# Kernel optimization log

Measured on AMD Instinct MI355X. Metric: run time of the kernel, lower is better.

Reference implementation:

```python
import jax, jax.numpy as jnp
import numpy as np

N = 100000
NNZ = 3200000
K = 3

def setup_inputs() -> dict:
    key = jax.random.key(0)
    ks = jax.random.split(key, 9)
    return {
        "x": jax.random.normal(ks[0], (N, 128), dtype=jnp.float32),
        "vals": jax.random.uniform(ks[1], (NNZ,), dtype=jnp.float32) * (1.0 / 32.0),
        "W1": jax.random.normal(ks[2], (128 * K, 256), dtype=jnp.float32) * 0.05,
        "b1": jax.random.normal(ks[3], (256,), dtype=jnp.float32) * 0.05,
        "W2": jax.random.normal(ks[4], (256 * K, 64), dtype=jnp.float32) * 0.05,
        "b2": jax.random.normal(ks[5], (64,), dtype=jnp.float32) * 0.05,
        "rows": jax.random.randint(ks[6], (NNZ,), 0, N, dtype=jnp.int32),
        "cols": jax.random.randint(ks[7], (NNZ,), 0, N, dtype=jnp.int32),
        "idx": jax.random.randint(ks[8], (50000,), 0, N, dtype=jnp.int32),
    }

def _spmm(rows, cols, vals, x):
    # sparse [N,N] @ dense [N,F] via gather + segment_sum
    return jax.ops.segment_sum(vals[:, None] * x[cols], rows, num_segments=N)

def _cheb_basis(x, rows, cols, vals, k):
    # Chebyshev recurrence: T0=x, T1=L x, T_m = 2 L T_{m-1} - T_{m-2}
    xs = [x]
    if k > 1:
        x0, x1 = x, _spmm(rows, cols, vals, x)
        xs.append(x1)
        for _ in range(2, k):
            x2 = 2.0 * _spmm(rows, cols, vals, x1) - x0
            xs.append(x2)
            x0, x1 = x1, x2
    # match torch layout: [N, F, K] -> [N, F*K] (per-feature K contiguous)
    return jnp.stack(xs, axis=2).reshape(x.shape[0], -1)

def reference(x, vals, W1, b1, W2, b2, rows, cols, idx):
    h = _cheb_basis(x, rows, cols, vals, K) @ W1 + b1
    h = jax.nn.relu(h)  # dropout omitted (eval mode)
    out = _cheb_basis(h, rows, cols, vals, K) @ W2 + b2
    return out[idx]
```

## Files before the change

kernel.cpp:

```cpp
#include <hip/hip_runtime.h>
#include <hip/hip_bf16.h>

typedef __attribute__((ext_vector_type(8))) __bf16 bf16x8;
typedef __attribute__((ext_vector_type(4))) float floatx4;
typedef unsigned short ushort_t;
typedef unsigned int uint_t;

#define N_NODES 100000
#define NNZ_E   3200000
#define N_IDX   50000
#define NB_BKT  196
#define PTILE   8192
#define PBLOCKS 391

__device__ __forceinline__ float bf2f(uint_t u16) {
  union { float f; uint_t i; } v; v.i = u16 << 16; return v.f;
}
__device__ __forceinline__ unsigned short f2bf(float f) {
  union { float f; uint_t i; } v; v.f = f;
  uint_t x = v.i;
  return (unsigned short)((x + 0x7FFFu + ((x >> 16) & 1u)) >> 16);
}


__global__ __launch_bounds__(256) void k_bhist(const int* __restrict__ rows,
                                               int* __restrict__ bcnt) {
  __shared__ int h[NB_BKT];
  for (int i = threadIdx.x; i < NB_BKT; i += 256) h[i] = 0;
  __syncthreads();
  int base = blockIdx.x * PTILE;
  for (int i = threadIdx.x; i < PTILE; i += 256) {
    int e = base + i;
    if (e < NNZ_E) atomicAdd(&h[rows[e] >> 9], 1);
  }
  __syncthreads();
  for (int i = threadIdx.x; i < NB_BKT; i += 256)
    if (h[i]) atomicAdd(&bcnt[i], h[i]);
}

__global__ void k_bscan(const int* __restrict__ bcnt, int* __restrict__ bbase,
                        int* __restrict__ bcur) {
  __shared__ int ts[256];
  int t = threadIdx.x;
  int v = (t < NB_BKT) ? bcnt[t] : 0;
  ts[t] = v;
  __syncthreads();
  for (int off = 1; off < 256; off <<= 1) {
    int x = ts[t];
    int a = (t >= off) ? ts[t - off] : 0;
    __syncthreads();
    ts[t] = x + a;
    __syncthreads();
  }
  if (t < NB_BKT) {
    int b = (t == 0) ? 0 : ts[t - 1];
    bbase[t] = b;
    bcur[t] = b;
  }
}

__global__ __launch_bounds__(256) void k_part(const int* __restrict__ rows,
                                              const int* __restrict__ cols,
                                              const float* __restrict__ vals,
                                              int* __restrict__ bcur,
                                              int2* __restrict__ tmp) {
  __shared__ int h[NB_BKT];
  for (int i = threadIdx.x; i < NB_BKT; i += 256) h[i] = 0;
  __syncthreads();
  int base = blockIdx.x * PTILE;
  for (int i = threadIdx.x; i < PTILE; i += 256) {
    int e = base + i;
    if (e < NNZ_E) atomicAdd(&h[rows[e] >> 9], 1);
  }
  __syncthreads();
  for (int i = threadIdx.x; i < NB_BKT; i += 256) {
    int c = h[i];
    h[i] = c ? atomicAdd(&bcur[i], c) : 0;
  }
  __syncthreads();
  for (int i = threadIdx.x; i < PTILE; i += 256) {
    int e = base + i;
    if (e < NNZ_E) {
      int rr = rows[e];
      int p = atomicAdd(&h[rr >> 9], 1);
      int2 o;
      o.x = cols[e] | ((rr & 511) << 17);
      o.y = __float_as_int(vals[e]);
      tmp[p] = o;
    }
  }
}

__global__ __launch_bounds__(512) void k_sort(const int* __restrict__ bbase,
                                              const int2* __restrict__ tmp,
                                              int2* __restrict__ edges,
                                              int* __restrict__ rowptr) {
  __shared__ int cnt[512];
  __shared__ int ts[512];
  int b = blockIdx.x, t = threadIdx.x;
  int s = bbase[b];
  int epos = (b == NB_BKT - 1) ? NNZ_E : bbase[b + 1];
  cnt[t] = 0;
  __syncthreads();
  for (int i = s + t; i < epos; i += 512)
    atomicAdd(&cnt[(tmp[i].x >> 17) & 511], 1);
  __syncthreads();
  ts[t] = cnt[t];
  __syncthreads();
  for (int off = 1; off < 512; off <<= 1) {
    int x = ts[t];
    int a = (t >= off) ? ts[t - off] : 0;
    __syncthreads();
    ts[t] = x + a;
    __syncthreads();
  }
  int pre = (t == 0) ? 0 : ts[t - 1];
  int grow = b * 512 + t;
  if (grow < N_NODES) rowptr[grow] = s + pre;
  cnt[t] = s + pre;
  __syncthreads();
  for (int i = s + t; i < epos; i += 512) {
    int2 p = tmp[i];
    int rl = (p.x >> 17) & 511;
    int pos = atomicAdd(&cnt[rl], 1);
    int2 o;
    o.x = p.x & 0x1FFFF;
    o.y = p.y;
    edges[pos] = o;
  }
  if (b == 0 && t == 0) rowptr[N_NODES] = NNZ_E;
}


__global__ void k_cvt(const float4* __restrict__ x, ushort4* __restrict__ xb) {
  int i = blockIdx.x * blockDim.x + threadIdx.x;
  if (i < N_NODES * 128 / 4) {
    float4 v = x[i];
    ushort4 o;
    o.x = f2bf(v.x); o.y = f2bf(v.y); o.z = f2bf(v.z); o.w = f2bf(v.w);
    xb[i] = o;
  }
}


__global__ void k_prepW1(const float* __restrict__ W, ushort_t* __restrict__ Wp) {
  int kp = blockIdx.x;
  int n  = threadIdx.x;
  int ch = kp >> 7;
  int f  = kp & 127;
  float v;
  if (ch == 0)      v = W[(f*3+0)*256+n] - W[(f*3+2)*256+n];
  else if (ch == 1) v = W[(f*3+1)*256+n];
  else              v = 2.0f * W[(f*3+2)*256+n];
  int kb = kp >> 5, kr = kp & 31;
  int lane = ((kr >> 3) << 4) | (n & 15);
  Wp[(((size_t)kb * 16 + (n >> 4)) * 64 + lane) * 8 + (kr & 7)] = f2bf(v);
}

__global__ void k_prepW2(const float* __restrict__ W, ushort_t* __restrict__ Wp) {
  int f = blockIdx.x;
  int c = threadIdx.x;
  int g = c >> 6, n = c & 63;
  float v;
  if (g == 0)      v = W[(f*3+0)*64+n] - W[(f*3+2)*64+n];
  else if (g == 1) v = W[(f*3+1)*64+n];
  else             v = 2.0f * W[(f*3+2)*64+n];
  int kb = f >> 5, kr = f & 31;
  int nb = c >> 4;
  int lane = ((kr >> 3) << 4) | (c & 15);
  Wp[(((size_t)kb * 12 + nb) * 64 + lane) * 8 + (kr & 7)] = f2bf(v);
}


__global__ __launch_bounds__(256) void k_spmm128(
    const int* __restrict__ rowptr, const int2* __restrict__ edges,
    const ushort_t* __restrict__ in, ushort_t* __restrict__ out) {
  int r = __builtin_amdgcn_readfirstlane(blockIdx.x * 4 + (threadIdx.x >> 6));
  int f = threadIdx.x & 63;
  int e0 = rowptr[r], e1 = rowptr[r + 1];
  float a0 = 0.f, a1 = 0.f;
  int e = e0;
  for (; e + 16 <= e1; e += 16) {
    int2 E[16];
#pragma unroll
    for (int j = 0; j < 16; ++j) E[j] = edges[e + j];
    uint_t q[16];
#pragma unroll
    for (int j = 0; j < 16; ++j)
      q[j] = *(const uint_t*)(in + (size_t)E[j].x * 128 + 2 * f);
#pragma unroll
    for (int j = 0; j < 16; ++j) {
      float v = __int_as_float(E[j].y);
      a0 = fmaf(v, bf2f(q[j] & 0xFFFFu), a0);
      a1 = fmaf(v, bf2f(q[j] >> 16), a1);
    }
  }
  for (; e + 4 <= e1; e += 4) {
    int2 E[4];
#pragma unroll
    for (int j = 0; j < 4; ++j) E[j] = edges[e + j];
    uint_t q[4];
#pragma unroll
    for (int j = 0; j < 4; ++j)
      q[j] = *(const uint_t*)(in + (size_t)E[j].x * 128 + 2 * f);
#pragma unroll
    for (int j = 0; j < 4; ++j) {
      float v = __int_as_float(E[j].y);
      a0 = fmaf(v, bf2f(q[j] & 0xFFFFu), a0);
      a1 = fmaf(v, bf2f(q[j] >> 16), a1);
    }
  }
  for (; e < e1; ++e) {
    int2 E = edges[e];
    uint_t q = *(const uint_t*)(in + (size_t)E.x * 128 + 2 * f);
    float v = __int_as_float(E.y);
    a0 = fmaf(v, bf2f(q & 0xFFFFu), a0);
    a1 = fmaf(v, bf2f(q >> 16), a1);
  }
  uint_t o = ((uint_t)f2bf(a1) << 16) | (uint_t)f2bf(a0);
  *(uint_t*)(out + (size_t)r * 128 + 2 * f) = o;
}


__global__ __launch_bounds__(256) void k_spmm64_add(
    const int* __restrict__ rowptr, const int2* __restrict__ edges,
    const ushort_t* __restrict__ p2, const ushort_t* __restrict__ p1,
    ushort_t* __restrict__ u) {
  int r = __builtin_amdgcn_readfirstlane(blockIdx.x * 4 + (threadIdx.x >> 6));
  int f = threadIdx.x & 63;
  int e0 = rowptr[r], e1 = rowptr[r + 1];
  float a = 0.f;
  int e = e0;
  for (; e + 16 <= e1; e += 16) {
    int2 E[16];
#pragma unroll
    for (int j = 0; j < 16; ++j) E[j] = edges[e + j];
    ushort_t q[16];
#pragma unroll
    for (int j = 0; j < 16; ++j) q[j] = p2[(size_t)E[j].x * 64 + f];
#pragma unroll
    for (int j = 0; j < 16; ++j)
      a = fmaf(__int_as_float(E[j].y), bf2f(q[j]), a);
  }
  for (; e + 4 <= e1; e += 4) {
    int2 E[4];
#pragma unroll
    for (int j = 0; j < 4; ++j) E[j] = edges[e + j];
    ushort_t q[4];
#pragma unroll
    for (int j = 0; j < 4; ++j) q[j] = p2[(size_t)E[j].x * 64 + f];
#pragma unroll
    for (int j = 0; j < 4; ++j)
      a = fmaf(__int_as_float(E[j].y), bf2f(q[j]), a);
  }
  for (; e < e1; ++e) {
    int2 E = edges[e];
    a = fmaf(__int_as_float(E.y), bf2f(p2[(size_t)E.x * 64 + f]), a);
  }
  float b = a + bf2f(p1[(size_t)r * 64 + f]);
  u[(size_t)r * 64 + f] = f2bf(b);
}


__global__ __launch_bounds__(256) void k_spmm64_idx(
    const int* __restrict__ rowptr, const int2* __restrict__ edges,
    const ushort_t* __restrict__ u, const float* __restrict__ p0,
    const int* __restrict__ idx, float* __restrict__ out) {
  int o = __builtin_amdgcn_readfirstlane(blockIdx.x * 4 + (threadIdx.x >> 6));
  int f = threadIdx.x & 63;
  int r = __builtin_amdgcn_readfirstlane(idx[o]);
  int e0 = rowptr[r], e1 = rowptr[r + 1];
  float a = 0.f;
  int e = e0;
  for (; e + 16 <= e1; e += 16) {
    int2 E[16];
#pragma unroll
    for (int j = 0; j < 16; ++j) E[j] = edges[e + j];
    ushort_t q[16];
#pragma unroll
    for (int j = 0; j < 16; ++j) q[j] = u[(size_t)E[j].x * 64 + f];
#pragma unroll
    for (int j = 0; j < 16; ++j)
      a = fmaf(__int_as_float(E[j].y), bf2f(q[j]), a);
  }
  for (; e + 4 <= e1; e += 4) {
    int2 E[4];
#pragma unroll
    for (int j = 0; j < 4; ++j) E[j] = edges[e + j];
    ushort_t q[4];
#pragma unroll
    for (int j = 0; j < 4; ++j) q[j] = u[(size_t)E[j].x * 64 + f];
#pragma unroll
    for (int j = 0; j < 4; ++j)
      a = fmaf(__int_as_float(E[j].y), bf2f(q[j]), a);
  }
  for (; e < e1; ++e) {
    int2 E = edges[e];
    a = fmaf(__int_as_float(E.y), bf2f(u[(size_t)E.x * 64 + f]), a);
  }
  float res = p0[(size_t)r * 64 + f] + a;
  out[(size_t)o * 64 + f] = res;
}


__global__ __launch_bounds__(256) void k_gemm1(
    const ushort_t* __restrict__ A0, const ushort_t* __restrict__ A1,
    const ushort_t* __restrict__ A2, const ushort_t* __restrict__ Bp,
    const float* __restrict__ bias, ushort_t* __restrict__ h) {
  int lane = threadIdx.x & 63;
  int ng = threadIdx.x >> 6;
  int r0 = blockIdx.x * 64;
  int mrl = lane & 15;
  int ko = (lane >> 4) << 3;
  floatx4 acc[4][4] = {};
#pragma unroll
  for (int kbg = 0; kbg < 12; ++kbg) {
    int c = kbg >> 2, kb = kbg & 3;
    const ushort_t* Asrc = (c == 0 ? A0 : c == 1 ? A1 : A2);
    bf16x8 a[4];
#pragma unroll
    for (int mi = 0; mi < 4; ++mi) {
      int mr = r0 + mi * 16 + mrl;
      if (mr > N_NODES - 1) mr = N_NODES - 1;
      a[mi] = *(const bf16x8*)(Asrc + (size_t)mr * 128 + kb * 32 + ko);
    }
    const ushort_t* Bb = Bp + (((size_t)(kbg * 16 + ng * 4)) * 64 + lane) * 8;
#pragma unroll
    for (int nt = 0; nt < 4; ++nt) {
      bf16x8 b = *(const bf16x8*)(Bb + (size_t)nt * 64 * 8);
#pragma unroll
      for (int mi = 0; mi < 4; ++mi)
        acc[mi][nt] = __builtin_amdgcn_mfma_f32_16x16x32_bf16(a[mi], b, acc[mi][nt], 0, 0, 0);
    }
  }
  int col0 = ng * 64 + (lane & 15);
  int rr0 = (lane >> 4) << 2;
#pragma unroll
  for (int nt = 0; nt < 4; ++nt) {
    int col = col0 + nt * 16;
    float bv = bias[col];
#pragma unroll
    for (int mi = 0; mi < 4; ++mi) {
      int rb = r0 + mi * 16 + rr0;
#pragma unroll
      for (int rg = 0; rg < 4; ++rg) {
        int row = rb + rg;
        if (row < N_NODES) {
          float v = acc[mi][nt][rg] + bv;
          v = v > 0.f ? v : 0.f;
          h[(size_t)row * 256 + col] = f2bf(v);
        }
      }
    }
  }
}


__global__ __launch_bounds__(256) void k_gemm2(
    const ushort_t* __restrict__ A, const ushort_t* __restrict__ Bp,
    const float* __restrict__ bias, float* __restrict__ p0,
    ushort_t* __restrict__ p1, ushort_t* __restrict__ p2) {
  int wid = (blockIdx.x * 256 + threadIdx.x) >> 6;
  int lane = threadIdx.x & 63;
  int mt4 = wid / 3, ng = wid - mt4 * 3;
  if (mt4 >= 1563) return;
  int r0 = mt4 * 64;
  int mrl = lane & 15;
  int ko = (lane >> 4) << 3;
  floatx4 acc[4][4] = {};
#pragma unroll
  for (int kb = 0; kb < 8; ++kb) {
    bf16x8 a[4];
#pragma unroll
    for (int mi = 0; mi < 4; ++mi) {
      int mr = r0 + mi * 16 + mrl;
      if (mr > N_NODES - 1) mr = N_NODES - 1;
      a[mi] = *(const bf16x8*)(A + (size_t)mr * 256 + kb * 32 + ko);
    }
    const ushort_t* Bb = Bp + (((size_t)(kb * 12 + ng * 4)) * 64 + lane) * 8;
#pragma unroll
    for (int nt = 0; nt < 4; ++nt) {
      bf16x8 b = *(const bf16x8*)(Bb + (size_t)nt * 64 * 8);
#pragma unroll
      for (int mi = 0; mi < 4; ++mi)
        acc[mi][nt] = __builtin_amdgcn_mfma_f32_16x16x32_bf16(a[mi], b, acc[mi][nt], 0, 0, 0);
    }
  }
  int c16 = lane & 15;
  int rr0 = (lane >> 4) << 2;
  if (ng == 0) {
#pragma unroll
    for (int nt = 0; nt < 4; ++nt) {
      float bv = bias[nt * 16 + c16];
#pragma unroll
      for (int mi = 0; mi < 4; ++mi) {
        int rb = r0 + mi * 16 + rr0;
#pragma unroll
        for (int rg = 0; rg < 4; ++rg) {
          int row = rb + rg;
          if (row < N_NODES)
            p0[(size_t)row * 64 + nt * 16 + c16] = acc[mi][nt][rg] + bv;
        }
      }
    }
  } else {
    ushort_t* dst = (ng == 1) ? p1 : p2;
#pragma unroll
    for (int nt = 0; nt < 4; ++nt)
#pragma unroll
      for (int mi = 0; mi < 4; ++mi) {
        int rb = r0 + mi * 16 + rr0;
#pragma unroll
        for (int rg = 0; rg < 4; ++rg) {
          int row = rb + rg;
          if (row < N_NODES)
            dst[(size_t)row * 64 + nt * 16 + c16] = f2bf(acc[mi][nt][rg]);
        }
      }
  }
}


extern "C" void kernel_launch(void* const* d_in, const int* in_sizes, int n_in,
                              void* d_out, int out_size, void* d_ws, size_t ws_size,
                              hipStream_t stream) {
  const float* x    = (const float*)d_in[0];
  const float* vals = (const float*)d_in[1];
  const float* W1   = (const float*)d_in[2];
  const float* b1   = (const float*)d_in[3];
  const float* W2   = (const float*)d_in[4];
  const float* b2   = (const float*)d_in[5];
  const int*   rows = (const int*)d_in[6];
  const int*   cols = (const int*)d_in[7];
  const int*   idx  = (const int*)d_in[8];
  float* out = (float*)d_out;

  char* w = (char*)d_ws;
  size_t off = 0;
  auto take = [&](size_t b) -> char* {
    char* p = w + off;
    off += (b + 255) & ~(size_t)255;
    return p;
  };
  int*      bcnt    = (int*)take((size_t)NB_BKT * 4);
  int*      bbase   = (int*)take((size_t)NB_BKT * 4);
  int*      bcur    = (int*)take((size_t)NB_BKT * 4);
  int*      rowptr  = (int*)take((size_t)(N_NODES + 1) * 4);
  int2*     tmp     = (int2*)take((size_t)NNZ_E * 8);
  int2*     edges   = (int2*)take((size_t)NNZ_E * 8);
  ushort_t* xb      = (ushort_t*)take((size_t)N_NODES * 128 * 2);
  ushort_t* T1a     = (ushort_t*)take((size_t)N_NODES * 128 * 2);
  ushort_t* U1      = (ushort_t*)take((size_t)N_NODES * 128 * 2);
  ushort_t* h       = (ushort_t*)take((size_t)N_NODES * 256 * 2);
  ushort_t* W1p     = (ushort_t*)take((size_t)384 * 256 * 2);
  ushort_t* W2p     = (ushort_t*)take((size_t)256 * 192 * 2);

  float*    p0 = (float*)xb;
  ushort_t* p1 = T1a;
  ushort_t* p2 = T1a + (size_t)N_NODES * 64;
  ushort_t* u  = U1;

  hipMemsetAsync(bcnt, 0, (size_t)NB_BKT * 4, stream);
  k_bhist<<<PBLOCKS, 256, 0, stream>>>(rows, bcnt);
  k_bscan<<<1, 256, 0, stream>>>(bcnt, bbase, bcur);
  k_part<<<PBLOCKS, 256, 0, stream>>>(rows, cols, vals, bcur, tmp);
  k_sort<<<NB_BKT, 512, 0, stream>>>(bbase, tmp, edges, rowptr);

  k_cvt<<<(N_NODES * 128 / 4 + 255) / 256, 256, 0, stream>>>((const float4*)x, (ushort4*)xb);
  k_prepW1<<<384, 256, 0, stream>>>(W1, W1p);
  k_prepW2<<<256, 192, 0, stream>>>(W2, W2p);

  k_spmm128<<<N_NODES / 4, 256, 0, stream>>>(rowptr, edges, xb, T1a);
  k_spmm128<<<N_NODES / 4, 256, 0, stream>>>(rowptr, edges, T1a, U1);
  k_gemm1<<<1563, 256, 0, stream>>>(xb, T1a, U1, W1p, b1, h);

  k_gemm2<<<1173, 256, 0, stream>>>(h, W2p, b2, p0, p1, p2);
  k_spmm64_add<<<N_NODES / 4, 256, 0, stream>>>(rowptr, edges, p2, p1, u);
  k_spmm64_idx<<<N_IDX / 4, 256, 0, stream>>>(rowptr, edges, u, p0, idx, out);
}
```

Measured before the change: 672.1 us.

## Replace two-pass bucket sort with per-row counting sort and fuse prep kernels

Builds the CSR with a per-row histogram using global atomics, a two-level scan, and a direct atomic scatter into the edges array. This removes the temporary buffer and the second local sort pass. The three conversion and weight-prep kernels are merged into one launch to cut launch overhead. The trade-off is heavy global atomic contention on row counters and fully scattered edge writes, with edge order within a row now nondeterministic.

Result: slower. 830.7 us (+23.6%).

```diff
diff --git a/kernel.cpp b/kernel.cpp
--- a/kernel.cpp
+++ b/kernel.cpp
@@ -10,8 +10,7 @@
 #define NNZ_E   3200000
 #define N_IDX   50000
 #define NB_BKT  196
-#define PTILE   8192
-#define PBLOCKS 391
+#define NROW_PAD (NB_BKT * 512)
 
 __device__ __forceinline__ float bf2f(uint_t u16) {
   union { float f; uint_t i; } v; v.i = u16 << 16; return v.f;
@@ -23,19 +22,27 @@
 }
 
 
-__global__ __launch_bounds__(256) void k_bhist(const int* __restrict__ rows,
-                                               int* __restrict__ bcnt) {
-  __shared__ int h[NB_BKT];
-  for (int i = threadIdx.x; i < NB_BKT; i += 256) h[i] = 0;
+__global__ __launch_bounds__(256) void k_rhist(const int4* __restrict__ rows,
+                                               int* __restrict__ rcnt) {
+  int i = blockIdx.x * 256 + threadIdx.x;
+  int4 r = rows[i];
+  atomicAdd(&rcnt[r.x], 1);
+  atomicAdd(&rcnt[r.y], 1);
+  atomicAdd(&rcnt[r.z], 1);
+  atomicAdd(&rcnt[r.w], 1);
+}
+
+__global__ __launch_bounds__(512) void k_rscan1(const int* __restrict__ rcnt,
+                                                int* __restrict__ bsum) {
+  __shared__ int s[512];
+  int t = threadIdx.x;
+  s[t] = rcnt[blockIdx.x * 512 + t];
   __syncthreads();
-  int base = blockIdx.x * PTILE;
-  for (int i = threadIdx.x; i < PTILE; i += 256) {
-    int e = base + i;
-    if (e < NNZ_E) atomicAdd(&h[rows[e] >> 9], 1);
-  }
-  __syncthreads();
-  for (int i = threadIdx.x; i < NB_BKT; i += 256)
-    if (h[i]) atomicAdd(&bcnt[i], h[i]);
+  for (int off = 256; off > 0; off >>= 1) {
+    if (t < off) s[t] += s[t + off];
+    __syncthreads();
+  }
+  if (t == 0) bsum[blockIdx.x] = s[0];
 }
 
 __global__ void k_bscan(const int* __restrict__ bcnt, int* __restrict__ bbase,
@@ -59,53 +66,14 @@
   }
 }
 
-__global__ __launch_bounds__(256) void k_part(const int* __restrict__ rows,
-                                              const int* __restrict__ cols,
-                                              const float* __restrict__ vals,
-                                              int* __restrict__ bcur,
-                                              int2* __restrict__ tmp) {
-  __shared__ int h[NB_BKT];
-  for (int i = threadIdx.x; i < NB_BKT; i += 256) h[i] = 0;
-  __syncthreads();
-  int base = blockIdx.x * PTILE;
-  for (int i = threadIdx.x; i < PTILE; i += 256) {
-    int e = base + i;
-    if (e < NNZ_E) atomicAdd(&h[rows[e] >> 9], 1);
-  }
-  __syncthreads();
-  for (int i = threadIdx.x; i < NB_BKT; i += 256) {
-    int c = h[i];
-    h[i] = c ? atomicAdd(&bcur[i], c) : 0;
-  }
-  __syncthreads();
-  for (int i = threadIdx.x; i < PTILE; i += 256) {
-    int e = base + i;
-    if (e < NNZ_E) {
-      int rr = rows[e];
-      int p = atomicAdd(&h[rr >> 9], 1);
-      int2 o;
-      o.x = cols[e] | ((rr & 511) << 17);
-      o.y = __float_as_int(vals[e]);
-      tmp[p] = o;
-    }
-  }
-}
-
-__global__ __launch_bounds__(512) void k_sort(const int* __restrict__ bbase,
-                                              const int2* __restrict__ tmp,
-                                              int2* __restrict__ edges,
-                                              int* __restrict__ rowptr) {
-  __shared__ int cnt[512];
+__global__ __launch_bounds__(512) void k_rscan2(const int* __restrict__ rcnt,
+                                                const int* __restrict__ bbase,
+                                                int* __restrict__ rowptr,
+                                                int* __restrict__ cur) {
   __shared__ int ts[512];
   int b = blockIdx.x, t = threadIdx.x;
-  int s = bbase[b];
-  int epos = (b == NB_BKT - 1) ? NNZ_E : bbase[b + 1];
-  cnt[t] = 0;
-  __syncthreads();
-  for (int i = s + t; i < epos; i += 512)
-    atomicAdd(&cnt[(tmp[i].x >> 17) & 511], 1);
-  __syncthreads();
-  ts[t] = cnt[t];
+  int g = b * 512 + t;
+  ts[t] = rcnt[g];
   __syncthreads();
   for (int off = 1; off < 512; off <<= 1) {
     int x = ts[t];
@@ -115,60 +83,69 @@
     __syncthreads();
   }
   int pre = (t == 0) ? 0 : ts[t - 1];
-  int grow = b * 512 + t;
-  if (grow < N_NODES) rowptr[grow] = s + pre;
-  cnt[t] = s + pre;
-  __syncthreads();
-  for (int i = s + t; i < epos; i += 512) {
-    int2 p = tmp[i];
-    int rl = (p.x >> 17) & 511;
-    int pos = atomicAdd(&cnt[rl], 1);
-    int2 o;
-    o.x = p.x & 0x1FFFF;
-    o.y = p.y;
-    edges[pos] = o;
-  }
-  if (b == 0 && t == 0) rowptr[N_NODES] = NNZ_E;
-}
-
-
-__global__ void k_cvt(const float4* __restrict__ x, ushort4* __restrict__ xb) {
-  int i = blockIdx.x * blockDim.x + threadIdx.x;
-  if (i < N_NODES * 128 / 4) {
+  int base = bbase[b] + pre;
+  if (g <= N_NODES) rowptr[g] = base;
+  if (g < N_NODES) cur[g] = base;
+}
+
+__global__ __launch_bounds__(256) void k_rscatter(const int4* __restrict__ rows,
+                                                  const int4* __restrict__ cols,
+                                                  const float4* __restrict__ vals,
+                                                  int* __restrict__ cur,
+                                                  int2* __restrict__ edges) {
+  int i = blockIdx.x * 256 + threadIdx.x;
+  int4 r = rows[i];
+  int4 c = cols[i];
+  float4 v = vals[i];
+  int p0 = atomicAdd(&cur[r.x], 1);
+  int p1 = atomicAdd(&cur[r.y], 1);
+  int p2 = atomicAdd(&cur[r.z], 1);
+  int p3 = atomicAdd(&cur[r.w], 1);
+  edges[p0] = make_int2(c.x, __float_as_int(v.x));
+  edges[p1] = make_int2(c.y, __float_as_int(v.y));
+  edges[p2] = make_int2(c.z, __float_as_int(v.z));
+  edges[p3] = make_int2(c.w, __float_as_int(v.w));
+}
+
+
+__global__ __launch_bounds__(256) void k_prep(
+    const float4* __restrict__ x, const float* __restrict__ W1,
+    const float* __restrict__ W2, ushort4* __restrict__ xb,
+    ushort_t* __restrict__ W1p, ushort_t* __restrict__ W2p) {
+  int b = blockIdx.x;
+  if (b < 12500) {
+    int i = b * 256 + threadIdx.x;
     float4 v = x[i];
     ushort4 o;
     o.x = f2bf(v.x); o.y = f2bf(v.y); o.z = f2bf(v.z); o.w = f2bf(v.w);
     xb[i] = o;
-  }
-}
-
-
-__global__ void k_prepW1(const float* __restrict__ W, ushort_t* __restrict__ Wp) {
-  int kp = blockIdx.x;
-  int n  = threadIdx.x;
-  int ch = kp >> 7;
-  int f  = kp & 127;
-  float v;
-  if (ch == 0)      v = W[(f*3+0)*256+n] - W[(f*3+2)*256+n];
-  else if (ch == 1) v = W[(f*3+1)*256+n];
-  else              v = 2.0f * W[(f*3+2)*256+n];
-  int kb = kp >> 5, kr = kp & 31;
-  int lane = ((kr >> 3) << 4) | (n & 15);
-  Wp[(((size_t)kb * 16 + (n >> 4)) * 64 + lane) * 8 + (kr & 7)] = f2bf(v);
-}
-
-__global__ void k_prepW2(const float* __restrict__ W, ushort_t* __restrict__ Wp) {
-  int f = blockIdx.x;
-  int c = threadIdx.x;
-  int g = c >> 6, n = c & 63;
-  float v;
-  if (g == 0)      v = W[(f*3+0)*64+n] - W[(f*3+2)*64+n];
-  else if (g == 1) v = W[(f*3+1)*64+n];
-  else             v = 2.0f * W[(f*3+2)*64+n];
-  int kb = f >> 5, kr = f & 31;
-  int nb = c >> 4;
-  int lane = ((kr >> 3) << 4) | (c & 15);
-  Wp[(((size_t)kb * 12 + nb) * 64 + lane) * 8 + (kr & 7)] = f2bf(v);
+  } else if (b < 12884) {
+    int kp = b - 12500;
+    int n  = threadIdx.x;
+    int ch = kp >> 7;
+    int f  = kp & 127;
+    float v;
+    if (ch == 0)      v = W1[(f*3+0)*256+n] - W1[(f*3+2)*256+n];
+    else if (ch == 1) v = W1[(f*3+1)*256+n];
+    else              v = 2.0f * W1[(f*3+2)*256+n];
+    int kb = kp >> 5, kr = kp & 31;
+    int lane = ((kr >> 3) << 4) | (n & 15);
+    W1p[(((size_t)kb * 16 + (n >> 4)) * 64 + lane) * 8 + (kr & 7)] = f2bf(v);
+  } else {
+    int f = b - 12884;
+    int c = threadIdx.x;
+    if (c < 192) {
+      int g = c >> 6, n = c & 63;
+      float v;
+      if (g == 0)      v = W2[(f*3+0)*64+n] - W2[(f*3+2)*64+n];
+      else if (g == 1) v = W2[(f*3+1)*64+n];
+      else             v = 2.0f * W2[(f*3+2)*64+n];
+      int kb = f >> 5, kr = f & 31;
+      int nb = c >> 4;
+      int lane = ((kr >> 3) << 4) | (c & 15);
+      W2p[(((size_t)kb * 12 + nb) * 64 + lane) * 8 + (kr & 7)] = f2bf(v);
+    }
+  }
 }
 
 
@@ -442,11 +419,12 @@
     off += (b + 255) & ~(size_t)255;
     return p;
   };
-  int*      bcnt    = (int*)take((size_t)NB_BKT * 4);
+  int*      rcnt    = (int*)take((size_t)NROW_PAD * 4);
+  int*      cur     = (int*)take((size_t)N_NODES * 4);
+  int*      bsum    = (int*)take((size_t)NB_BKT * 4);
   int*      bbase   = (int*)take((size_t)NB_BKT * 4);
-  int*      bcur    = (int*)take((size_t)NB_BKT * 4);
+  int*      bcur_d  = (int*)take((size_t)NB_BKT * 4);
   int*      rowptr  = (int*)take((size_t)(N_NODES + 1) * 4);
-  int2*     tmp     = (int2*)take((size_t)NNZ_E * 8);
   int2*     edges   = (int2*)take((size_t)NNZ_E * 8);
   ushort_t* xb      = (ushort_t*)take((size_t)N_NODES * 128 * 2);
   ushort_t* T1a     = (ushort_t*)take((size_t)N_NODES * 128 * 2);
@@ -460,15 +438,15 @@
   ushort_t* p2 = T1a + (size_t)N_NODES * 64;
   ushort_t* u  = U1;
 
-  hipMemsetAsync(bcnt, 0, (size_t)NB_BKT * 4, stream);
-  k_bhist<<<PBLOCKS, 256, 0, stream>>>(rows, bcnt);
-  k_bscan<<<1, 256, 0, stream>>>(bcnt, bbase, bcur);
-  k_part<<<PBLOCKS, 256, 0, stream>>>(rows, cols, vals, bcur, tmp);
-  k_sort<<<NB_BKT, 512, 0, stream>>>(bbase, tmp, edges, rowptr);
-
-  k_cvt<<<(N_NODES * 128 / 4 + 255) / 256, 256, 0, stream>>>((const float4*)x, (ushort4*)xb);
-  k_prepW1<<<384, 256, 0, stream>>>(W1, W1p);
-  k_prepW2<<<256, 192, 0, stream>>>(W2, W2p);
+  hipMemsetAsync(rcnt, 0, (size_t)NROW_PAD * 4, stream);
+  k_rhist<<<NNZ_E / 4 / 256, 256, 0, stream>>>((const int4*)rows, rcnt);
+  k_rscan1<<<NB_BKT, 512, 0, stream>>>(rcnt, bsum);
+  k_bscan<<<1, 256, 0, stream>>>(bsum, bbase, bcur_d);
+  k_rscan2<<<NB_BKT, 512, 0, stream>>>(rcnt, bbase, rowptr, cur);
+  k_rscatter<<<NNZ_E / 4 / 256, 256, 0, stream>>>((const int4*)rows, (const int4*)cols,
+                                                  (const float4*)vals, cur, edges);
+
+  k_prep<<<13140, 256, 0, stream>>>((const float4*)x, W1, W2, (ushort4*)xb, W1p, W2p);
 
   k_spmm128<<<N_NODES / 4, 256, 0, stream>>>(rowptr, edges, xb, T1a);
   k_spmm128<<<N_NODES / 4, 256, 0, stream>>>(rowptr, edges, T1a, U1);
```

## Split wave halves across edges in 64-wide SpMM and merge prep kernels

Applied to the files above, without the earlier changes.

The two 64-feature SpMM kernels now have each half-wave handle alternating edges, loading two bf16 features per lane as a 32-bit word, then combine the halves with a cross-lane shuffle. This doubles the bytes per gather instruction and halves the serial edge loop length per lane. The three small preprocessing kernels (x conversion and the two weight repacks) are merged into one launch to cut launch overhead. The cost is extra shuffle and select work, and half of the lanes sit idle during the final store.

Result: no change. 675.3 us (+0.5%).

```diff
diff --git a/kernel.cpp b/kernel.cpp
--- a/kernel.cpp
+++ b/kernel.cpp
@@ -20,6 +20,9 @@
   union { float f; uint_t i; } v; v.f = f;
   uint_t x = v.i;
   return (unsigned short)((x + 0x7FFFu + ((x >> 16) & 1u)) >> 16);
+}
+__device__ __forceinline__ uint_t pk(float lo, float hi) {
+  return ((uint_t)f2bf(hi) << 16) | (uint_t)f2bf(lo);
 }
 
 
@@ -132,43 +135,44 @@
 }
 
 
-__global__ void k_cvt(const float4* __restrict__ x, ushort4* __restrict__ xb) {
-  int i = blockIdx.x * blockDim.x + threadIdx.x;
-  if (i < N_NODES * 128 / 4) {
+__global__ __launch_bounds__(256) void k_prep(
+    const float4* __restrict__ x, const float* __restrict__ W1,
+    const float* __restrict__ W2, ushort4* __restrict__ xb,
+    ushort_t* __restrict__ W1p, ushort_t* __restrict__ W2p) {
+  int b = blockIdx.x;
+  if (b < 12500) {
+    int i = b * 256 + threadIdx.x;
     float4 v = x[i];
     ushort4 o;
     o.x = f2bf(v.x); o.y = f2bf(v.y); o.z = f2bf(v.z); o.w = f2bf(v.w);
     xb[i] = o;
-  }
-}
-
-
-__global__ void k_prepW1(const float* __restrict__ W, ushort_t* __restrict__ Wp) {
-  int kp = blockIdx.x;
-  int n  = threadIdx.x;
-  int ch = kp >> 7;
-  int f  = kp & 127;
-  float v;
-  if (ch == 0)      v = W[(f*3+0)*256+n] - W[(f*3+2)*256+n];
-  else if (ch == 1) v = W[(f*3+1)*256+n];
-  else              v = 2.0f * W[(f*3+2)*256+n];
-  int kb = kp >> 5, kr = kp & 31;
-  int lane = ((kr >> 3) << 4) | (n & 15);
-  Wp[(((size_t)kb * 16 + (n >> 4)) * 64 + lane) * 8 + (kr & 7)] = f2bf(v);
-}
-
-__global__ void k_prepW2(const float* __restrict__ W, ushort_t* __restrict__ Wp) {
-  int f = blockIdx.x;
-  int c = threadIdx.x;
-  int g = c >> 6, n = c & 63;
-  float v;
-  if (g == 0)      v = W[(f*3+0)*64+n] - W[(f*3+2)*64+n];
-  else if (g == 1) v = W[(f*3+1)*64+n];
-  else             v = 2.0f * W[(f*3+2)*64+n];
-  int kb = f >> 5, kr = f & 31;
-  int nb = c >> 4;
-  int lane = ((kr >> 3) << 4) | (c & 15);
-  Wp[(((size_t)kb * 12 + nb) * 64 + lane) * 8 + (kr & 7)] = f2bf(v);
+  } else if (b < 12884) {
+    int kp = b - 12500;
+    int n  = threadIdx.x;
+    int ch = kp >> 7;
+    int f  = kp & 127;
+    float v;
+    if (ch == 0)      v = W1[(f*3+0)*256+n] - W1[(f*3+2)*256+n];
+    else if (ch == 1) v = W1[(f*3+1)*256+n];
+    else              v = 2.0f * W1[(f*3+2)*256+n];
+    int kb = kp >> 5, kr = kp & 31;
+    int lane = ((kr >> 3) << 4) | (n & 15);
+    W1p[(((size_t)kb * 16 + (n >> 4)) * 64 + lane) * 8 + (kr & 7)] = f2bf(v);
+  } else {
+    int f = b - 12884;
+    int c = threadIdx.x;
+    if (c < 192) {
+      int g = c >> 6, n = c & 63;
+      float v;
+      if (g == 0)      v = W2[(f*3+0)*64+n] - W2[(f*3+2)*64+n];
+      else if (g == 1) v = W2[(f*3+1)*64+n];
+      else             v = 2.0f * W2[(f*3+2)*64+n];
+      int kb = f >> 5, kr = f & 31;
+      int nb = c >> 4;
+      int lane = ((kr >> 3) << 4) | (c & 15);
+      W2p[(((size_t)kb * 12 + nb) * 64 + lane) * 8 + (kr & 7)] = f2bf(v);
+    }
+  }
 }
 
 
@@ -227,38 +231,51 @@
     const ushort_t* __restrict__ p2, const ushort_t* __restrict__ p1,
     ushort_t* __restrict__ u) {
   int r = __builtin_amdgcn_readfirstlane(blockIdx.x * 4 + (threadIdx.x >> 6));
-  int f = threadIdx.x & 63;
+  int lane = threadIdx.x & 63;
+  int half = lane >> 5, l5 = lane & 31;
   int e0 = rowptr[r], e1 = rowptr[r + 1];
-  float a = 0.f;
+  float a0 = 0.f, a1 = 0.f;
   int e = e0;
   for (; e + 16 <= e1; e += 16) {
-    int2 E[16];
-#pragma unroll
-    for (int j = 0; j < 16; ++j) E[j] = edges[e + j];
-    ushort_t q[16];
-#pragma unroll
-    for (int j = 0; j < 16; ++j) q[j] = p2[(size_t)E[j].x * 64 + f];
-#pragma unroll
-    for (int j = 0; j < 16; ++j)
-      a = fmaf(__int_as_float(E[j].y), bf2f(q[j]), a);
-  }
-  for (; e + 4 <= e1; e += 4) {
-    int2 E[4];
-#pragma unroll
-    for (int j = 0; j < 4; ++j) E[j] = edges[e + j];
-    ushort_t q[4];
-#pragma unroll
-    for (int j = 0; j < 4; ++j) q[j] = p2[(size_t)E[j].x * 64 + f];
-#pragma unroll
-    for (int j = 0; j < 4; ++j)
-      a = fmaf(__int_as_float(E[j].y), bf2f(q[j]), a);
-  }
-  for (; e < e1; ++e) {
-    int2 E = edges[e];
-    a = fmaf(__int_as_float(E.y), bf2f(p2[(size_t)E.x * 64 + f]), a);
-  }
-  float b = a + bf2f(p1[(size_t)r * 64 + f]);
-  u[(size_t)r * 64 + f] = f2bf(b);
+    int2 Ea[8], Eb[8];
+#pragma unroll
+    for (int j = 0; j < 8; ++j) { Ea[j] = edges[e + 2*j]; Eb[j] = edges[e + 2*j + 1]; }
+    uint_t q[8];
+#pragma unroll
+    for (int j = 0; j < 8; ++j) {
+      int c = half ? Eb[j].x : Ea[j].x;
+      q[j] = *(const uint_t*)(p2 + (size_t)c * 64 + 2 * l5);
+    }
+#pragma unroll
+    for (int j = 0; j < 8; ++j) {
+      float v = __int_as_float(half ? Eb[j].y : Ea[j].y);
+      a0 = fmaf(v, bf2f(q[j] & 0xFFFFu), a0);
+      a1 = fmaf(v, bf2f(q[j] >> 16), a1);
+    }
+  }
+  for (; e + 2 <= e1; e += 2) {
+    int2 Ea = edges[e], Eb = edges[e + 1];
+    int c = half ? Eb.x : Ea.x;
+    uint_t q = *(const uint_t*)(p2 + (size_t)c * 64 + 2 * l5);
+    float v = __int_as_float(half ? Eb.y : Ea.y);
+    a0 = fmaf(v, bf2f(q & 0xFFFFu), a0);
+    a1 = fmaf(v, bf2f(q >> 16), a1);
+  }
+  if (e < e1) {
+    int2 Ea = edges[e];
+    uint_t q = *(const uint_t*)(p2 + (size_t)Ea.x * 64 + 2 * l5);
+    float v = half ? 0.f : __int_as_float(Ea.y);
+    a0 = fmaf(v, bf2f(q & 0xFFFFu), a0);
+    a1 = fmaf(v, bf2f(q >> 16), a1);
+  }
+  a0 += __shfl_xor(a0, 32);
+  a1 += __shfl_xor(a1, 32);
+  if (half == 0) {
+    uint_t pp = *(const uint_t*)(p1 + (size_t)r * 64 + 2 * l5);
+    float b0 = a0 + bf2f(pp & 0xFFFFu);
+    float b1 = a1 + bf2f(pp >> 16);
+    *(uint_t*)(u + (size_t)r * 64 + 2 * l5) = pk(b0, b1);
+  }
 }
 
 
@@ -267,39 +284,51 @@
     const ushort_t* __restrict__ u, const float* __restrict__ p0,
     const int* __restrict__ idx, float* __restrict__ out) {
   int o = __builtin_amdgcn_readfirstlane(blockIdx.x * 4 + (threadIdx.x >> 6));
-  int f = threadIdx.x & 63;
+  int lane = threadIdx.x & 63;
+  int half = lane >> 5, l5 = lane & 31;
   int r = __builtin_amdgcn_readfirstlane(idx[o]);
   int e0 = rowptr[r], e1 = rowptr[r + 1];
-  float a = 0.f;
+  float a0 = 0.f, a1 = 0.f;
   int e = e0;
   for (; e + 16 <= e1; e += 16) {
-    int2 E[16];
-#pragma unroll
-    for (int j = 0; j < 16; ++j) E[j] = edges[e + j];
-    ushort_t q[16];
-#pragma unroll
-    for (int j = 0; j < 16; ++j) q[j] = u[(size_t)E[j].x * 64 + f];
-#pragma unroll
-    for (int j = 0; j < 16; ++j)
-      a = fmaf(__int_as_float(E[j].y), bf2f(q[j]), a);
-  }
-  for (; e + 4 <= e1; e += 4) {
-    int2 E[4];
-#pragma unroll
-    for (int j = 0; j < 4; ++j) E[j] = edges[e + j];
-    ushort_t q[4];
-#pragma unroll
-    for (int j = 0; j < 4; ++j) q[j] = u[(size_t)E[j].x * 64 + f];
-#pragma unroll
-    for (int j = 0; j < 4; ++j)
-      a = fmaf(__int_as_float(E[j].y), bf2f(q[j]), a);
-  }
-  for (; e < e1; ++e) {
-    int2 E = edges[e];
-    a = fmaf(__int_as_float(E.y), bf2f(u[(size_t)E.x * 64 + f]), a);
-  }
-  float res = p0[(size_t)r * 64 + f] + a;
-  out[(size_t)o * 64 + f] = res;
+    int2 Ea[8], Eb[8];
+#pragma unroll
+    for (int j = 0; j < 8; ++j) { Ea[j] = edges[e + 2*j]; Eb[j] = edges[e + 2*j + 1]; }
+    uint_t q[8];
+#pragma unroll
+    for (int j = 0; j < 8; ++j) {
+      int c = half ? Eb[j].x : Ea[j].x;
+      q[j] = *(const uint_t*)(u + (size_t)c * 64 + 2 * l5);
+    }
+#pragma unroll
+    for (int j = 0; j < 8; ++j) {
+      float v = __int_as_float(half ? Eb[j].y : Ea[j].y);
+      a0 = fmaf(v, bf2f(q[j] & 0xFFFFu), a0);
+      a1 = fmaf(v, bf2f(q[j] >> 16), a1);
+    }
+  }
+  for (; e + 2 <= e1; e += 2) {
+    int2 Ea = edges[e], Eb = edges[e + 1];
+    int c = half ? Eb.x : Ea.x;
+    uint_t q = *(const uint_t*)(u + (size_t)c * 64 + 2 * l5);
+    float v = __int_as_float(half ? Eb.y : Ea.y);
+    a0 = fmaf(v, bf2f(q & 0xFFFFu), a0);
+    a1 = fmaf(v, bf2f(q >> 16), a1);
+  }
+  if (e < e1) {
+    int2 Ea = edges[e];
+    uint_t q = *(const uint_t*)(u + (size_t)Ea.x * 64 + 2 * l5);
+    float v = half ? 0.f : __int_as_float(Ea.y);
+    a0 = fmaf(v, bf2f(q & 0xFFFFu), a0);
+    a1 = fmaf(v, bf2f(q >> 16), a1);
+  }
+  a0 += __shfl_xor(a0, 32);
+  a1 += __shfl_xor(a1, 32);
+  if (half == 0) {
+    float2 b = *(const float2*)(p0 + (size_t)r * 64 + 2 * l5);
+    float2 ww; ww.x = b.x + a0; ww.y = b.y + a1;
+    *(float2*)(out + (size_t)o * 64 + 2 * l5) = ww;
+  }
 }
 
 
@@ -466,9 +495,7 @@
   k_part<<<PBLOCKS, 256, 0, stream>>>(rows, cols, vals, bcur, tmp);
   k_sort<<<NB_BKT, 512, 0, stream>>>(bbase, tmp, edges, rowptr);
 
-  k_cvt<<<(N_NODES * 128 / 4 + 255) / 256, 256, 0, stream>>>((const float4*)x, (ushort4*)xb);
-  k_prepW1<<<384, 256, 0, stream>>>(W1, W1p);
-  k_prepW2<<<256, 192, 0, stream>>>(W2, W2p);
+  k_prep<<<13140, 256, 0, stream>>>((const float4*)x, W1, W2, (ushort4*)xb, W1p, W2p);
 
   k_spmm128<<<N_NODES / 4, 256, 0, stream>>>(rowptr, edges, xb, T1a);
   k_spmm128<<<N_NODES / 4, 256, 0, stream>>>(rowptr, edges, T1a, U1);
```
